# Optimization experiments

Measured on AMD Instinct MI355X. Metric: run time of the kernel, lower is better.

The kernel has to match this reference:

```python
import jax, jax.numpy as jnp
import numpy as np

B, N, T, H = 32, 16, 64, 256


def setup_inputs() -> dict:
    key = jax.random.key(0)
    k1, k2, k3 = jax.random.split(key, 3)
    node_rnn_output = jax.random.normal(k1, (B, T, H), dtype=jnp.float32)
    neigh_rnn_output = jax.random.normal(k2, (B, N, T, H), dtype=jnp.float32)
    # neighbor counts in [1, N] to avoid divide-by-zero in 1/sqrt scaling
    neighbors_number = jax.random.randint(k3, (B,), 1, N + 1, dtype=jnp.int64)
    return {
        "node_rnn_output": node_rnn_output,
        "neigh_rnn_output": neigh_rnn_output,
        "neighbors_number": neighbors_number,
    }


def reference(node_rnn_output, neigh_rnn_output, neighbors_number):
    b, t, h = node_rnn_output.shape
    n = neigh_rnn_output.shape[1]
    # [B, N*T, H]
    flat_neigh = neigh_rnn_output.reshape(b, n * t, h)
    # repeat node output along time axis: [B, N*T, H]
    stacked_node = jnp.tile(node_rnn_output, (1, n, 1))
    # S = flat_neigh @ stacked_node^T : [B, N*T, N*T]
    S = jnp.einsum("bqh,bkh->bqk", flat_neigh, stacked_node)
    scale = jnp.sqrt(neighbors_number.astype(S.dtype))  # [B]
    S = S / scale[:, None, None]
    A = jax.nn.softmax(S, axis=-1)
    # dropout with p=0 (eval / reference) is identity
    W = A.sum(axis=1).reshape(b, n, t)  # [B, N, T]
    output = jnp.einsum("bqk,bkh->bqh", A, flat_neigh)  # [B, N*T, H]
    return (output, W)
```

## Files before the change

kernel.cpp:

```cpp
#include <hip/hip_runtime.h>

#define Bc  32
#define Nc  16
#define Tc  64
#define Hc  256
#define NTc 1024

typedef unsigned short u16;
using v8s = __attribute__((ext_vector_type(8))) short;
using v4f = __attribute__((ext_vector_type(4))) float;

static __device__ __forceinline__ u16 f2bf(float x) {
    unsigned u = __float_as_uint(x);
    unsigned r = u + 0x7fffu + ((u >> 16) & 1u);
    return (u16)(r >> 16);
}
static __device__ __forceinline__ float bf2f(u16 h) {
    return __uint_as_float(((unsigned)h) << 16);
}

__global__ __launch_bounds__(256) void prep_kernel(const float* __restrict__ neigh,
                                                   const float* __restrict__ node,
                                                   u16* __restrict__ MT,
                                                   u16* __restrict__ NH,
                                                   u16* __restrict__ NL,
                                                   float* __restrict__ Wsum) {
    __shared__ float Ls[64][68];
    int bk = blockIdx.x, tid = threadIdx.x;

    if (bk < 128) {
        int b = bk >> 2, h0 = (bk & 3) << 6;
#pragma unroll
        for (int rep = 0; rep < 4; rep++) {
            int idx = rep * 256 + tid;
            int t = idx >> 4, c4 = idx & 15;
            const float4* p = (const float4*)(neigh + ((size_t)b * Nc * Tc + t) * Hc + h0) + c4;
            float4 a = make_float4(0.f, 0.f, 0.f, 0.f);
#pragma unroll
            for (int i = 0; i < Nc; i++) {
                float4 v = p[(size_t)i * (Tc * Hc / 4)];
                a.x += v.x; a.y += v.y; a.z += v.z; a.w += v.w;
            }
            const float r = 1.0f / 16.0f;
            Ls[t][c4 * 4 + 0] = a.x * r;
            Ls[t][c4 * 4 + 1] = a.y * r;
            Ls[t][c4 * 4 + 2] = a.z * r;
            Ls[t][c4 * 4 + 3] = a.w * r;
        }
        __syncthreads();
#pragma unroll
        for (int rep = 0; rep < 4; rep++) {
            int idx = rep * 256 + tid;
            int h = idx >> 4, t4 = idx & 15;
            ushort4 o;
            o.x = f2bf(Ls[t4 * 4 + 0][h]);
            o.y = f2bf(Ls[t4 * 4 + 1][h]);
            o.z = f2bf(Ls[t4 * 4 + 2][h]);
            o.w = f2bf(Ls[t4 * 4 + 3][h]);
            *(ushort4*)(MT + ((size_t)b * Hc + h0 + h) * Tc + t4 * 4) = o;
        }
    } else {
        int b = bk - 128;
#pragma unroll
        for (int rep = 0; rep < 16; rep++) {
            int idx = rep * 256 + tid;
            int t = idx >> 6, c4 = idx & 63;
            size_t off = ((size_t)b * Tc + t) * Hc + c4 * 4;
            float4 v = *(const float4*)(node + off);
            ushort4 hs, ls;
            hs.x = f2bf(v.x); ls.x = f2bf(v.x - bf2f(hs.x));
            hs.y = f2bf(v.y); ls.y = f2bf(v.y - bf2f(hs.y));
            hs.z = f2bf(v.z); ls.z = f2bf(v.z - bf2f(hs.z));
            hs.w = f2bf(v.w); ls.w = f2bf(v.w - bf2f(hs.w));
            *(ushort4*)(NH + off) = hs;
            *(ushort4*)(NL + off) = ls;
        }
        if (tid < 64) Wsum[b * 64 + tid] = 0.f;
    }
}

__global__ __launch_bounds__(256, 2) void fused_kernel(const float* __restrict__ neigh,
                                                       const u16* __restrict__ NH,
                                                       const u16* __restrict__ NL,
                                                       const int* __restrict__ nbr,
                                                       const u16* __restrict__ MT,
                                                       float* __restrict__ out,
                                                       float* __restrict__ Wsum) {
    __shared__ u16 Xh[64][72];
    __shared__ u16 Xl[64][72];
    __shared__ u16 Nh[64][72];
    __shared__ u16 Nl[64][72];
    __shared__ u16 Ph[64][72];
    __shared__ float Wtmp[256];

    int b  = blockIdx.x >> 4;
    int i  = blockIdx.x & 15;
    int q0 = i << 6;

    int tid  = threadIdx.x;
    int w    = tid >> 6;
    int lane = tid & 63;
    int quad = lane >> 4;
    int c    = lane & 15;

    int nb = (nbr[1] == 0) ? nbr[2 * b] : nbr[b];
    float rscale = rsqrtf((float)nb);

    const float* Xg  = neigh + ((size_t)b * Nc * Tc + q0) * Hc;
    const u16*   NHg = NH + (size_t)b * Tc * Hc;
    const u16*   NLg = NL + (size_t)b * Tc * Hc;
    const u16*   MTg = MT + (size_t)b * Hc * Tc;

    v4f acc[4];
#pragma unroll
    for (int nt = 0; nt < 4; nt++)
#pragma unroll
        for (int rg = 0; rg < 4; rg++) acc[nt][rg] = 0.f;

    for (int k0 = 0; k0 < Hc; k0 += 64) {
#pragma unroll
        for (int rep = 0; rep < 4; rep++) {
            int idx = rep * 256 + tid;
            int row = idx >> 4, c4 = idx & 15;
            float4 xv = *(const float4*)(Xg + (size_t)row * Hc + k0 + c4 * 4);
            ushort4 hs, ls;
            hs.x = f2bf(xv.x); ls.x = f2bf(xv.x - bf2f(hs.x));
            hs.y = f2bf(xv.y); ls.y = f2bf(xv.y - bf2f(hs.y));
            hs.z = f2bf(xv.z); ls.z = f2bf(xv.z - bf2f(hs.z));
            hs.w = f2bf(xv.w); ls.w = f2bf(xv.w - bf2f(hs.w));
            *(ushort4*)&Xh[row][c4 * 4] = hs;
            *(ushort4*)&Xl[row][c4 * 4] = ls;
        }
#pragma unroll
        for (int rep = 0; rep < 2; rep++) {
            int idx = rep * 256 + tid;
            int row = idx >> 3, c8 = idx & 7;
            *(uint4*)&Nh[row][c8 * 8] = *(const uint4*)(NHg + (size_t)row * Hc + k0 + c8 * 8);
            *(uint4*)&Nl[row][c8 * 8] = *(const uint4*)(NLg + (size_t)row * Hc + k0 + c8 * 8);
        }
        __syncthreads();

#pragma unroll
        for (int ks = 0; ks < 64; ks += 32) {
            v8s ah = *(const v8s*)&Xh[w * 16 + c][ks + quad * 8];
            v8s al = *(const v8s*)&Xl[w * 16 + c][ks + quad * 8];
#pragma unroll
            for (int nt = 0; nt < 4; nt++) {
                v8s bh = *(const v8s*)&Nh[nt * 16 + c][ks + quad * 8];
                v8s bl = *(const v8s*)&Nl[nt * 16 + c][ks + quad * 8];
                acc[nt] = __builtin_amdgcn_mfma_f32_16x16x32_bf16(ah, bh, acc[nt], 0, 0, 0);
                acc[nt] = __builtin_amdgcn_mfma_f32_16x16x32_bf16(ah, bl, acc[nt], 0, 0, 0);
                acc[nt] = __builtin_amdgcn_mfma_f32_16x16x32_bf16(al, bh, acc[nt], 0, 0, 0);
            }
        }
        __syncthreads();
    }

#pragma unroll
    for (int nt = 0; nt < 4; nt++)
#pragma unroll
        for (int rg = 0; rg < 4; rg++) acc[nt][rg] *= rscale;

#pragma unroll
    for (int rg = 0; rg < 4; rg++) {
        float m = fmaxf(fmaxf(acc[0][rg], acc[1][rg]), fmaxf(acc[2][rg], acc[3][rg]));
#pragma unroll
        for (int d = 1; d < 16; d <<= 1) m = fmaxf(m, __shfl_xor(m, d));
        float e0 = __expf(acc[0][rg] - m);
        float e1 = __expf(acc[1][rg] - m);
        float e2 = __expf(acc[2][rg] - m);
        float e3 = __expf(acc[3][rg] - m);
        float s = e0 + e1 + e2 + e3;
#pragma unroll
        for (int d = 1; d < 16; d <<= 1) s += __shfl_xor(s, d);
        float inv = 1.0f / s;
        acc[0][rg] = e0 * inv; acc[1][rg] = e1 * inv;
        acc[2][rg] = e2 * inv; acc[3][rg] = e3 * inv;
    }

#pragma unroll
    for (int nt = 0; nt < 4; nt++) {
        float cs = acc[nt][0] + acc[nt][1] + acc[nt][2] + acc[nt][3];
        cs += __shfl_xor(cs, 16);
        cs += __shfl_xor(cs, 32);
        if (quad == 0) Wtmp[w * 64 + nt * 16 + c] = cs;
    }

#pragma unroll
    for (int nt = 0; nt < 4; nt++)
#pragma unroll
        for (int rg = 0; rg < 4; rg++)
            Ph[w * 16 + quad * 4 + rg][nt * 16 + c] = f2bf(acc[nt][rg]);

    __syncthreads();

    if (tid < 64) {
        float s = Wtmp[tid] + Wtmp[64 + tid] + Wtmp[128 + tid] + Wtmp[192 + tid];
        atomicAdd(&Wsum[b * Tc + tid], s);
    }

    v8s pa0 = *(const v8s*)&Ph[w * 16 + c][quad * 8];
    v8s pa1 = *(const v8s*)&Ph[w * 16 + c][32 + quad * 8];

    for (int h0 = 0; h0 < Hc; h0 += 64) {
#pragma unroll
        for (int rep = 0; rep < 2; rep++) {
            int idx = rep * 256 + tid;
            int row = idx >> 3, c8 = idx & 7;
            *(uint4*)&Xh[row][c8 * 8] = *(const uint4*)(MTg + (size_t)(h0 + row) * Tc + c8 * 8);
        }
        __syncthreads();

        v4f oc[4];
#pragma unroll
        for (int ht = 0; ht < 4; ht++)
#pragma unroll
            for (int rg = 0; rg < 4; rg++) oc[ht][rg] = 0.f;

#pragma unroll
        for (int ht = 0; ht < 4; ht++) {
            v8s b0 = *(const v8s*)&Xh[ht * 16 + c][quad * 8];
            v8s b1 = *(const v8s*)&Xh[ht * 16 + c][32 + quad * 8];
            oc[ht] = __builtin_amdgcn_mfma_f32_16x16x32_bf16(pa0, b0, oc[ht], 0, 0, 0);
            oc[ht] = __builtin_amdgcn_mfma_f32_16x16x32_bf16(pa1, b1, oc[ht], 0, 0, 0);
        }

        float* ob = out + ((size_t)b * NTc + q0 + w * 16 + quad * 4) * Hc + h0 + c;
#pragma unroll
        for (int ht = 0; ht < 4; ht++)
#pragma unroll
            for (int rg = 0; rg < 4; rg++)
                ob[(size_t)rg * Hc + ht * 16] = oc[ht][rg];

        __syncthreads();
    }
}

__global__ __launch_bounds__(256) void wexp_kernel(const float* __restrict__ Wsum,
                                                   float* __restrict__ Wout) {
    int idx = blockIdx.x * 256 + threadIdx.x;
    int b = idx >> 10;
    int t = idx & 63;
    Wout[idx] = Wsum[b * Tc + t] * (1.0f / 16.0f);
}

extern "C" void kernel_launch(void* const* d_in, const int* in_sizes, int n_in,
                              void* d_out, int out_size, void* d_ws, size_t ws_size,
                              hipStream_t stream) {
    const float* node  = (const float*)d_in[0];
    const float* neigh = (const float*)d_in[1];
    const int*   nbr   = (const int*)d_in[2];

    float* out = (float*)d_out;

    u16* MTw = (u16*)d_ws;
    u16* NHw = MTw + (size_t)Bc * Hc * Tc;
    u16* NLw = NHw + (size_t)Bc * Tc * Hc;
    float* Ww = (float*)(NLw + (size_t)Bc * Tc * Hc);

    prep_kernel <<<160, 256, 0, stream>>>(neigh, node, MTw, NHw, NLw, Ww);
    fused_kernel<<<512, 256, 0, stream>>>(neigh, NHw, NLw, nbr, MTw, out, Ww);
    wexp_kernel <<<128, 256, 0, stream>>>(Ww, out + (size_t)Bc * NTc * Hc);
}
```

Baseline: 106.5 us.

## Load MFMA operands straight from global memory and split prep kernel finer

The fused kernel drops its LDS staging tiles and block barriers for the QK and PV products. Each wave now reads its fragments directly from global memory (fp32 neighbour rows split on the fly, bf16 NH/NL/MT from cache). This removes shared-memory traffic and synchronisation, at the cost of redundant, less coalesced global and L2 reads across waves. The prep kernel is also split into 512 smaller blocks, one per 16-timestep slice, to expose more parallelism for the neighbour-mean reduction.

```diff
diff --git a/kernel.cpp b/kernel.cpp
--- a/kernel.cpp
+++ b/kernel.cpp
@@ -25,42 +25,38 @@
                                                    u16* __restrict__ NH,
                                                    u16* __restrict__ NL,
                                                    float* __restrict__ Wsum) {
-    __shared__ float Ls[64][68];
+    __shared__ float Ls[16][68];
     int bk = blockIdx.x, tid = threadIdx.x;
 
-    if (bk < 128) {
-        int b = bk >> 2, h0 = (bk & 3) << 6;
-#pragma unroll
-        for (int rep = 0; rep < 4; rep++) {
-            int idx = rep * 256 + tid;
-            int t = idx >> 4, c4 = idx & 15;
-            const float4* p = (const float4*)(neigh + ((size_t)b * Nc * Tc + t) * Hc + h0) + c4;
-            float4 a = make_float4(0.f, 0.f, 0.f, 0.f);
-#pragma unroll
-            for (int i = 0; i < Nc; i++) {
-                float4 v = p[(size_t)i * (Tc * Hc / 4)];
-                a.x += v.x; a.y += v.y; a.z += v.z; a.w += v.w;
-            }
-            const float r = 1.0f / 16.0f;
-            Ls[t][c4 * 4 + 0] = a.x * r;
-            Ls[t][c4 * 4 + 1] = a.y * r;
-            Ls[t][c4 * 4 + 2] = a.z * r;
-            Ls[t][c4 * 4 + 3] = a.w * r;
-        }
+    if (bk < 512) {
+        int b  = bk >> 4;
+        int h0 = ((bk >> 2) & 3) << 6;
+        int t0 = (bk & 3) << 4;
+        int t  = tid >> 4;
+        int h4 = tid & 15;
+        const float4* p = (const float4*)(neigh + ((size_t)(b * Nc * Tc) + (t0 + t)) * Hc + h0) + h4;
+        float4 a = make_float4(0.f, 0.f, 0.f, 0.f);
+#pragma unroll
+        for (int i = 0; i < Nc; i++) {
+            float4 v = p[(size_t)i * (Tc * Hc / 4)];
+            a.x += v.x; a.y += v.y; a.z += v.z; a.w += v.w;
+        }
+        const float r = 1.0f / 16.0f;
+        Ls[t][h4 * 4 + 0] = a.x * r;
+        Ls[t][h4 * 4 + 1] = a.y * r;
+        Ls[t][h4 * 4 + 2] = a.z * r;
+        Ls[t][h4 * 4 + 3] = a.w * r;
         __syncthreads();
-#pragma unroll
-        for (int rep = 0; rep < 4; rep++) {
-            int idx = rep * 256 + tid;
-            int h = idx >> 4, t4 = idx & 15;
-            ushort4 o;
-            o.x = f2bf(Ls[t4 * 4 + 0][h]);
-            o.y = f2bf(Ls[t4 * 4 + 1][h]);
-            o.z = f2bf(Ls[t4 * 4 + 2][h]);
-            o.w = f2bf(Ls[t4 * 4 + 3][h]);
-            *(ushort4*)(MT + ((size_t)b * Hc + h0 + h) * Tc + t4 * 4) = o;
-        }
+        int h  = tid >> 2;
+        int t4 = tid & 3;
+        ushort4 o;
+        o.x = f2bf(Ls[t4 * 4 + 0][h]);
+        o.y = f2bf(Ls[t4 * 4 + 1][h]);
+        o.z = f2bf(Ls[t4 * 4 + 2][h]);
+        o.w = f2bf(Ls[t4 * 4 + 3][h]);
+        *(ushort4*)(MT + ((size_t)b * Hc + h0 + h) * Tc + t0 + t4 * 4) = o;
     } else {
-        int b = bk - 128;
+        int b = bk - 512;
 #pragma unroll
         for (int rep = 0; rep < 16; rep++) {
             int idx = rep * 256 + tid;
@@ -86,10 +82,6 @@
                                                        const u16* __restrict__ MT,
                                                        float* __restrict__ out,
                                                        float* __restrict__ Wsum) {
-    __shared__ u16 Xh[64][72];
-    __shared__ u16 Xl[64][72];
-    __shared__ u16 Nh[64][72];
-    __shared__ u16 Nl[64][72];
     __shared__ u16 Ph[64][72];
     __shared__ float Wtmp[256];
 
@@ -106,10 +98,10 @@
     int nb = (nbr[1] == 0) ? nbr[2 * b] : nbr[b];
     float rscale = rsqrtf((float)nb);
 
-    const float* Xg  = neigh + ((size_t)b * Nc * Tc + q0) * Hc;
-    const u16*   NHg = NH + (size_t)b * Tc * Hc;
-    const u16*   NLg = NL + (size_t)b * Tc * Hc;
-    const u16*   MTg = MT + (size_t)b * Hc * Tc;
+    const float* Xrow = neigh + ((size_t)(b * Nc * Tc) + q0 + w * 16 + c) * Hc;
+    const u16*   NHb  = NH + (size_t)b * Tc * Hc;
+    const u16*   NLb  = NL + (size_t)b * Tc * Hc;
+    const u16*   MTb  = MT + (size_t)b * Hc * Tc;
 
     v4f acc[4];
 #pragma unroll
@@ -117,43 +109,30 @@
 #pragma unroll
         for (int rg = 0; rg < 4; rg++) acc[nt][rg] = 0.f;
 
-    for (int k0 = 0; k0 < Hc; k0 += 64) {
-#pragma unroll
-        for (int rep = 0; rep < 4; rep++) {
-            int idx = rep * 256 + tid;
-            int row = idx >> 4, c4 = idx & 15;
-            float4 xv = *(const float4*)(Xg + (size_t)row * Hc + k0 + c4 * 4);
-            ushort4 hs, ls;
-            hs.x = f2bf(xv.x); ls.x = f2bf(xv.x - bf2f(hs.x));
-            hs.y = f2bf(xv.y); ls.y = f2bf(xv.y - bf2f(hs.y));
-            hs.z = f2bf(xv.z); ls.z = f2bf(xv.z - bf2f(hs.z));
-            hs.w = f2bf(xv.w); ls.w = f2bf(xv.w - bf2f(hs.w));
-            *(ushort4*)&Xh[row][c4 * 4] = hs;
-            *(ushort4*)&Xl[row][c4 * 4] = ls;
-        }
-#pragma unroll
-        for (int rep = 0; rep < 2; rep++) {
-            int idx = rep * 256 + tid;
-            int row = idx >> 3, c8 = idx & 7;
-            *(uint4*)&Nh[row][c8 * 8] = *(const uint4*)(NHg + (size_t)row * Hc + k0 + c8 * 8);
-            *(uint4*)&Nl[row][c8 * 8] = *(const uint4*)(NLg + (size_t)row * Hc + k0 + c8 * 8);
-        }
-        __syncthreads();
-
-#pragma unroll
-        for (int ks = 0; ks < 64; ks += 32) {
-            v8s ah = *(const v8s*)&Xh[w * 16 + c][ks + quad * 8];
-            v8s al = *(const v8s*)&Xl[w * 16 + c][ks + quad * 8];
-#pragma unroll
-            for (int nt = 0; nt < 4; nt++) {
-                v8s bh = *(const v8s*)&Nh[nt * 16 + c][ks + quad * 8];
-                v8s bl = *(const v8s*)&Nl[nt * 16 + c][ks + quad * 8];
-                acc[nt] = __builtin_amdgcn_mfma_f32_16x16x32_bf16(ah, bh, acc[nt], 0, 0, 0);
-                acc[nt] = __builtin_amdgcn_mfma_f32_16x16x32_bf16(ah, bl, acc[nt], 0, 0, 0);
-                acc[nt] = __builtin_amdgcn_mfma_f32_16x16x32_bf16(al, bh, acc[nt], 0, 0, 0);
-            }
-        }
-        __syncthreads();
+#pragma unroll
+    for (int ks = 0; ks < Hc; ks += 32) {
+        float4 f0 = *(const float4*)(Xrow + ks + quad * 8);
+        float4 f1 = *(const float4*)(Xrow + ks + quad * 8 + 4);
+        v8s ah, al;
+        {
+            u16 h0 = f2bf(f0.x), h1 = f2bf(f0.y), h2 = f2bf(f0.z), h3 = f2bf(f0.w);
+            u16 h4 = f2bf(f1.x), h5 = f2bf(f1.y), h6 = f2bf(f1.z), h7 = f2bf(f1.w);
+            ah[0] = (short)h0; ah[1] = (short)h1; ah[2] = (short)h2; ah[3] = (short)h3;
+            ah[4] = (short)h4; ah[5] = (short)h5; ah[6] = (short)h6; ah[7] = (short)h7;
+            al[0] = (short)f2bf(f0.x - bf2f(h0)); al[1] = (short)f2bf(f0.y - bf2f(h1));
+            al[2] = (short)f2bf(f0.z - bf2f(h2)); al[3] = (short)f2bf(f0.w - bf2f(h3));
+            al[4] = (short)f2bf(f1.x - bf2f(h4)); al[5] = (short)f2bf(f1.y - bf2f(h5));
+            al[6] = (short)f2bf(f1.z - bf2f(h6)); al[7] = (short)f2bf(f1.w - bf2f(h7));
+        }
+#pragma unroll
+        for (int nt = 0; nt < 4; nt++) {
+            size_t roff = (size_t)(nt * 16 + c) * Hc + ks + quad * 8;
+            v8s bh = *(const v8s*)(NHb + roff);
+            v8s bl = *(const v8s*)(NLb + roff);
+            acc[nt] = __builtin_amdgcn_mfma_f32_16x16x32_bf16(ah, bh, acc[nt], 0, 0, 0);
+            acc[nt] = __builtin_amdgcn_mfma_f32_16x16x32_bf16(ah, bl, acc[nt], 0, 0, 0);
+            acc[nt] = __builtin_amdgcn_mfma_f32_16x16x32_bf16(al, bh, acc[nt], 0, 0, 0);
+        }
     }
 
 #pragma unroll
@@ -202,37 +181,19 @@
     v8s pa0 = *(const v8s*)&Ph[w * 16 + c][quad * 8];
     v8s pa1 = *(const v8s*)&Ph[w * 16 + c][32 + quad * 8];
 
-    for (int h0 = 0; h0 < Hc; h0 += 64) {
-#pragma unroll
-        for (int rep = 0; rep < 2; rep++) {
-            int idx = rep * 256 + tid;
-            int row = idx >> 3, c8 = idx & 7;
-            *(uint4*)&Xh[row][c8 * 8] = *(const uint4*)(MTg + (size_t)(h0 + row) * Tc + c8 * 8);
-        }
-        __syncthreads();
-
-        v4f oc[4];
-#pragma unroll
-        for (int ht = 0; ht < 4; ht++)
-#pragma unroll
-            for (int rg = 0; rg < 4; rg++) oc[ht][rg] = 0.f;
-
-#pragma unroll
-        for (int ht = 0; ht < 4; ht++) {
-            v8s b0 = *(const v8s*)&Xh[ht * 16 + c][quad * 8];
-            v8s b1 = *(const v8s*)&Xh[ht * 16 + c][32 + quad * 8];
-            oc[ht] = __builtin_amdgcn_mfma_f32_16x16x32_bf16(pa0, b0, oc[ht], 0, 0, 0);
-            oc[ht] = __builtin_amdgcn_mfma_f32_16x16x32_bf16(pa1, b1, oc[ht], 0, 0, 0);
-        }
-
-        float* ob = out + ((size_t)b * NTc + q0 + w * 16 + quad * 4) * Hc + h0 + c;
-#pragma unroll
-        for (int ht = 0; ht < 4; ht++)
-#pragma unroll
-            for (int rg = 0; rg < 4; rg++)
-                ob[(size_t)rg * Hc + ht * 16] = oc[ht][rg];
-
-        __syncthreads();
+    float* ob = out + ((size_t)b * NTc + q0 + w * 16 + quad * 4) * Hc + c;
+#pragma unroll
+    for (int ht = 0; ht < 16; ht++) {
+        const u16* mr = MTb + (size_t)(ht * 16 + c) * Tc;
+        v8s b0 = *(const v8s*)(mr + quad * 8);
+        v8s b1 = *(const v8s*)(mr + 32 + quad * 8);
+        v4f oc;
+        oc[0] = 0.f; oc[1] = 0.f; oc[2] = 0.f; oc[3] = 0.f;
+        oc = __builtin_amdgcn_mfma_f32_16x16x32_bf16(pa0, b0, oc, 0, 0, 0);
+        oc = __builtin_amdgcn_mfma_f32_16x16x32_bf16(pa1, b1, oc, 0, 0, 0);
+#pragma unroll
+        for (int rg = 0; rg < 4; rg++)
+            ob[(size_t)rg * Hc + ht * 16] = oc[rg];
     }
 }
 
@@ -258,7 +219,7 @@
     u16* NLw = NHw + (size_t)Bc * Tc * Hc;
     float* Ww = (float*)(NLw + (size_t)Bc * Tc * Hc);
 
-    prep_kernel <<<160, 256, 0, stream>>>(neigh, node, MTw, NHw, NLw, Ww);
+    prep_kernel <<<544, 256, 0, stream>>>(neigh, node, MTw, NHw, NLw, Ww);
     fused_kernel<<<512, 256, 0, stream>>>(neigh, NHw, NLw, nbr, MTw, out, Ww);
     wexp_kernel <<<128, 256, 0, stream>>>(Ww, out + (size_t)Bc * NTc * Hc);
 }
```

Result: slower. 121.0 us (+13.6%).
